# Performance work log

Measured on AMD Instinct MI355X. Metric: run time of the kernel, lower is better.

## Reference

```python
import jax, jax.numpy as jnp
import numpy as np

B = 500_000      # batch rows
F = 100          # fixed by x.view(-1, 100)
NT = 10          # number of tails (clusters)
C = 10           # cluster size (features per tail)
H = 7            # hidden = ceil(0.75 * C)


def setup_inputs() -> dict:
    key = jax.random.key(0)
    ks = jax.random.split(key, 7)
    x = jax.random.normal(ks[0], (B, F), dtype=jnp.float32)
    Wt = jax.random.normal(ks[1], (NT, H, C), dtype=jnp.float32) * 0.1
    hbias_t = jax.random.normal(ks[2], (NT, H), dtype=jnp.float32) * 0.1
    vbias_t = jax.random.normal(ks[3], (NT, C), dtype=jnp.float32) * 0.1
    Wh = jax.random.normal(ks[4], (H, NT), dtype=jnp.float32) * 0.1
    hbias_h = jax.random.normal(ks[5], (H,), dtype=jnp.float32) * 0.1
    vbias_h = jax.random.normal(ks[6], (NT,), dtype=jnp.float32) * 0.1
    clusters = jnp.arange(F, dtype=jnp.int32).reshape(NT, C)
    return {"x": x, "Wt": Wt, "hbias_t": hbias_t, "vbias_t": vbias_t,
            "Wh": Wh, "hbias_h": hbias_h, "vbias_h": vbias_h,
            "clusters": clusters}


def reference(x, Wt, hbias_t, vbias_t, Wh, hbias_h, vbias_h, clusters):
    x = x.reshape(-1, F)
    # fused gather: [B, NT, C]
    xc = x[:, clusters]
    # tail encoders: z = xc @ We.T + hbias  (We = Wt[t], shape [H, C])
    z = jnp.einsum('btc,thc->bth', xc, Wt) + hbias_t[None]          # [B, NT, H]
    # tail decoders (tied weights W.T): out = z @ We + vbias
    out = jnp.einsum('bth,thc->btc', z, Wt) + vbias_t[None]          # [B, NT, C]
    # per-sample, per-tail RMSE then log
    rmse = jnp.sqrt(jnp.mean((out - xc) ** 2, axis=-1))              # [B, NT]
    tails = jnp.log(rmse)                                            # [B, NT]
    # head autoencoder over tail scores
    zh = tails @ Wh.T + hbias_h                                      # [B, H]
    head_out = zh @ Wh + vbias_h                                     # [B, NT]
    return head_out, tails
```

## Files before the change

kernel.cpp:

```cpp
#include <hip/hip_runtime.h>


typedef float v2f __attribute__((ext_vector_type(2)));

constexpr int F  = 100;
constexpr int NT = 10;
constexpr int C  = 10;
constexpr int H  = 7;
constexpr int BLOCK = 512;
constexpr int RPB   = 64;
constexpr int XSTR  = 101;

__device__ __forceinline__ int tail_col(int t) {
    return (t < 8) ? 10 * t : 10 * (t - 8) + 1;
}
__device__ __forceinline__ int head_col(int c) {
    return (c < 8) ? 2 + c : 4 + c;
}

__device__ __forceinline__ void do_tile(
    int t,
    float* __restrict__ xrow,
    const float* __restrict__ Wt,
    const float* __restrict__ hbt,
    const float* __restrict__ vbt)
{
    const int cb = t * 10;
    v2f xc[5];
    #pragma unroll
    for (int c2 = 0; c2 < 5; ++c2) {
        xc[c2].x = xrow[cb + 2 * c2];
        xc[c2].y = xrow[cb + 2 * c2 + 1];
    }
    v2f out[5];
    #pragma unroll
    for (int c2 = 0; c2 < 5; ++c2) {
        out[c2].x = vbt[t * C + 2 * c2];
        out[c2].y = vbt[t * C + 2 * c2 + 1];
    }
    #pragma unroll
    for (int h = 0; h < H; ++h) {
        v2f w[5];
        #pragma unroll
        for (int c2 = 0; c2 < 5; ++c2) {
            w[c2].x = Wt[(t * H + h) * C + 2 * c2];
            w[c2].y = Wt[(t * H + h) * C + 2 * c2 + 1];
        }
        v2f za; za.x = hbt[t * H + h]; za.y = 0.f;
        #pragma unroll
        for (int c2 = 0; c2 < 5; ++c2)
            za = __builtin_elementwise_fma(xc[c2], w[c2], za);
        const float z = za.x + za.y;
        v2f zz; zz.x = z; zz.y = z;
        #pragma unroll
        for (int c2 = 0; c2 < 5; ++c2)
            out[c2] = __builtin_elementwise_fma(zz, w[c2], out[c2]);
    }
    v2f a2; a2.x = 0.f; a2.y = 0.f;
    #pragma unroll
    for (int c2 = 0; c2 < 5; ++c2) {
        const v2f d = out[c2] - xc[c2];
        a2 = __builtin_elementwise_fma(d, d, a2);
    }
    const float acc = a2.x + a2.y;
    xrow[tail_col(t)] = 0.5f * __logf(acc * 0.1f);
}

__global__ __launch_bounds__(BLOCK, 8) void kitnet_main(
    const float* __restrict__ x,
    const float* __restrict__ Wt,
    const float* __restrict__ hbt,
    const float* __restrict__ vbt,
    const float* __restrict__ Wh,
    const float* __restrict__ hbh,
    const float* __restrict__ vbh,
    float* __restrict__ head_out,
    float* __restrict__ tails_out,
    int B)
{
    __shared__ float xs[RPB * XSTR];

    const int tid = threadIdx.x;
    const long long r0 = (long long)blockIdx.x * RPB;
    const int nrows = (int)min((long long)RPB, (long long)B - r0);

    {
        const float4* __restrict__ xg = (const float4*)(x + r0 * F);
        const int n4 = nrows * (F / 4);
        #pragma unroll
        for (int k = 0; k < (RPB * F / 4 + BLOCK - 1) / BLOCK; ++k) {
            const int idx = tid + k * BLOCK;
            if (idx < n4) {
                float4 v = xg[idx];
                const int row  = idx / 25;
                const int feat = (idx - row * 25) * 4;
                float* d = &xs[row * XSTR + feat];
                d[0] = v.x; d[1] = v.y; d[2] = v.z; d[3] = v.w;
            }
        }
    }
    __syncthreads();

    const int lane = tid & 63;
    const int wave = __builtin_amdgcn_readfirstlane(tid >> 6);
    float* xrow = &xs[lane * XSTR];

    do_tile(wave, xrow, Wt, hbt, vbt);
    if (wave < 2) do_tile(8 + wave, xrow, Wt, hbt, vbt);
    __syncthreads();

    if (tid < RPB) {
        float* trow = &xs[tid * XSTR];
        float tl[NT];
        #pragma unroll
        for (int t = 0; t < NT; ++t) tl[t] = trow[tail_col(t)];
        float zh[H];
        #pragma unroll
        for (int h = 0; h < H; ++h) {
            float s = hbh[h];
            #pragma unroll
            for (int t = 0; t < NT; ++t) s = fmaf(tl[t], Wh[h * NT + t], s);
            zh[h] = s;
        }
        #pragma unroll
        for (int c = 0; c < NT; ++c) {
            float s = vbh[c];
            #pragma unroll
            for (int h = 0; h < H; ++h) s = fmaf(zh[h], Wh[h * NT + c], s);
            trow[head_col(c)] = s;
        }
    }
    __syncthreads();

    const int nout = nrows * NT;
    float* __restrict__ ho = head_out  + r0 * NT;
    float* __restrict__ to = tails_out + r0 * NT;
    #pragma unroll
    for (int k0 = 0; k0 < (RPB * NT + BLOCK - 1) / BLOCK; ++k0) {
        const int k = tid + k0 * BLOCK;
        if (k < nout) {
            const int row = k / 10;
            const int c   = k - row * 10;
            ho[k] = xs[row * XSTR + head_col(c)];
            to[k] = xs[row * XSTR + tail_col(c)];
        }
    }
}

extern "C" void kernel_launch(void* const* d_in, const int* in_sizes, int n_in,
                              void* d_out, int out_size, void* d_ws, size_t ws_size,
                              hipStream_t stream) {
    const float* x   = (const float*)d_in[0];
    const float* Wt  = (const float*)d_in[1];
    const float* hbt = (const float*)d_in[2];
    const float* vbt = (const float*)d_in[3];
    const float* Wh  = (const float*)d_in[4];
    const float* hbh = (const float*)d_in[5];
    const float* vbh = (const float*)d_in[6];
    const int B = in_sizes[0] / F;
    float* head  = (float*)d_out;
    float* tails = head + (size_t)B * NT;
    const int grid = (B + RPB - 1) / RPB;
    kitnet_main<<<grid, BLOCK, 0, stream>>>(x, Wt, hbt, vbt, Wh, hbh, vbh,
                                            head, tails, B);
}
```

Measured before the change: 304.6 us.

## Parallelize head stage across 320 threads and store outputs directly with nontemporal writes

Changes the shared-memory row stride to an even value so x rows can be read and written as 2-float vectors in LDS, and switches the global x load to a nontemporal vector load. The head autoencoder now spreads each row over 5 threads that each produce two outputs, instead of 64 threads doing the whole row. Those threads write head and tail outputs straight to global memory with nontemporal v2 stores, which removes one __syncthreads and the separate copy-out pass. The head stage now recomputes zh redundantly in each of the 5 threads, and the even stride may add LDS bank conflicts.

Measured after the change: 292.0 us, median of 2. 1.04x faster.

```diff
diff --git a/kernel.cpp b/kernel.cpp
--- a/kernel.cpp
+++ b/kernel.cpp
@@ -2,6 +2,7 @@
 
 
 typedef float v2f __attribute__((ext_vector_type(2)));
+typedef float v4f __attribute__((ext_vector_type(4)));
 
 constexpr int F  = 100;
 constexpr int NT = 10;
@@ -9,13 +10,10 @@
 constexpr int H  = 7;
 constexpr int BLOCK = 512;
 constexpr int RPB   = 64;
-constexpr int XSTR  = 101;
+constexpr int XSTR  = 102;
 
 __device__ __forceinline__ int tail_col(int t) {
     return (t < 8) ? 10 * t : 10 * (t - 8) + 1;
-}
-__device__ __forceinline__ int head_col(int c) {
-    return (c < 8) ? 2 + c : 4 + c;
 }
 
 __device__ __forceinline__ void do_tile(
@@ -26,12 +24,11 @@
     const float* __restrict__ vbt)
 {
     const int cb = t * 10;
+    const v2f* __restrict__ xr2 = (const v2f*)(xrow + cb);
     v2f xc[5];
     #pragma unroll
-    for (int c2 = 0; c2 < 5; ++c2) {
-        xc[c2].x = xrow[cb + 2 * c2];
-        xc[c2].y = xrow[cb + 2 * c2 + 1];
-    }
+    for (int c2 = 0; c2 < 5; ++c2) xc[c2] = xr2[c2];
+
     v2f out[5];
     #pragma unroll
     for (int c2 = 0; c2 < 5; ++c2) {
@@ -85,17 +82,19 @@
     const int nrows = (int)min((long long)RPB, (long long)B - r0);
 
     {
-        const float4* __restrict__ xg = (const float4*)(x + r0 * F);
+        const v4f* __restrict__ xg = (const v4f*)(x + r0 * F);
         const int n4 = nrows * (F / 4);
         #pragma unroll
         for (int k = 0; k < (RPB * F / 4 + BLOCK - 1) / BLOCK; ++k) {
             const int idx = tid + k * BLOCK;
             if (idx < n4) {
-                float4 v = xg[idx];
+                v4f v = __builtin_nontemporal_load(&xg[idx]);
                 const int row  = idx / 25;
                 const int feat = (idx - row * 25) * 4;
-                float* d = &xs[row * XSTR + feat];
-                d[0] = v.x; d[1] = v.y; d[2] = v.z; d[3] = v.w;
+                v2f* d = (v2f*)&xs[row * XSTR + feat];
+                v2f lo; lo.x = v.x; lo.y = v.y;
+                v2f hi; hi.x = v.z; hi.y = v.w;
+                d[0] = lo; d[1] = hi;
             }
         }
     }
@@ -109,8 +108,11 @@
     if (wave < 2) do_tile(8 + wave, xrow, Wt, hbt, vbt);
     __syncthreads();
 
-    if (tid < RPB) {
-        float* trow = &xs[tid * XSTR];
+    const int ntask = nrows * 5;
+    if (tid < ntask) {
+        const int row = tid / 5;
+        const int c0  = (tid - row * 5) * 2;
+        const float* __restrict__ trow = &xs[row * XSTR];
         float tl[NT];
         #pragma unroll
         for (int t = 0; t < NT; ++t) tl[t] = trow[tail_col(t)];
@@ -122,28 +124,17 @@
             for (int t = 0; t < NT; ++t) s = fmaf(tl[t], Wh[h * NT + t], s);
             zh[h] = s;
         }
+        float h0 = vbh[c0], h1 = vbh[c0 + 1];
         #pragma unroll
-        for (int c = 0; c < NT; ++c) {
-            float s = vbh[c];
-            #pragma unroll
-            for (int h = 0; h < H; ++h) s = fmaf(zh[h], Wh[h * NT + c], s);
-            trow[head_col(c)] = s;
+        for (int h = 0; h < H; ++h) {
+            h0 = fmaf(zh[h], Wh[h * NT + c0],     h0);
+            h1 = fmaf(zh[h], Wh[h * NT + c0 + 1], h1);
         }
-    }
-    __syncthreads();
-
-    const int nout = nrows * NT;
-    float* __restrict__ ho = head_out  + r0 * NT;
-    float* __restrict__ to = tails_out + r0 * NT;
-    #pragma unroll
-    for (int k0 = 0; k0 < (RPB * NT + BLOCK - 1) / BLOCK; ++k0) {
-        const int k = tid + k0 * BLOCK;
-        if (k < nout) {
-            const int row = k / 10;
-            const int c   = k - row * 10;
-            ho[k] = xs[row * XSTR + head_col(c)];
-            to[k] = xs[row * XSTR + tail_col(c)];
-        }
+        const long long o = (r0 + row) * NT + c0;
+        v2f hv; hv.x = h0; hv.y = h1;
+        v2f tv; tv.x = trow[tail_col(c0)]; tv.y = trow[tail_col(c0 + 1)];
+        __builtin_nontemporal_store(hv, (v2f*)(head_out  + o));
+        __builtin_nontemporal_store(tv, (v2f*)(tails_out + o));
     }
 }
 
```
